# Performance work log

Hardware: AMD Instinct MI355X
Metric: run time of the kernel (lower is better)

## Reference

```python
import jax, jax.numpy as jnp
import numpy as np

B, N, DM, H, FF = 8, 2048, 1024, 16, 4096
D = DM // H // 2  # head_dim = 32
LAMBDA_INIT = 0.8 - 0.6 * float(np.exp(-0.3 * 1.0))  # layer_num=1


def _layernorm(x, g, b, eps=1e-5):
    mu = jnp.mean(x, axis=-1, keepdims=True)
    var = jnp.mean(jnp.square(x - mu), axis=-1, keepdims=True)
    return (x - mu) * jax.lax.rsqrt(var + eps) * g + b


def _rmsnorm(x, eps=1e-5):
    return x * jax.lax.rsqrt(jnp.mean(x * x, axis=-1, keepdims=True) + eps)


def _diff_attn(x, Wq, Wk, Wv, lq1, lq2, lk1, lk2, Wo, bo):
    b, n, d = x.shape
    scale = D ** -0.5
    # rearrange 'b n (h d q) -> b n (q h) d'
    q = (x @ Wq.T).reshape(b, n, H, D, 2).transpose(0, 1, 4, 2, 3).reshape(b, n, 2 * H, D) * scale
    k = (x @ Wk.T).reshape(b, n, H, D, 2).transpose(0, 1, 4, 2, 3).reshape(b, n, 2 * H, D)
    # rearrange 'b n (h d) -> b h n d' with d = 2*head_dim
    v = (x @ Wv.T).reshape(b, n, H, 2 * D).transpose(0, 2, 1, 3)
    # per-position head-vs-head scores: [b, n, 2H, 2H]
    att = jnp.einsum('bnqd,bnkd->bnqk', q, k)
    att = jnp.nan_to_num(att)
    att = jax.nn.softmax(att.astype(jnp.float32), axis=-1)
    lam = jnp.exp(jnp.sum(lq1 * lk1)) - jnp.exp(jnp.sum(lq2 * lk2)) + LAMBDA_INIT
    # rearrange 'b n (q h) (k a) -> q k b n h a'; take [0,0] - lam*[1,1]
    att6 = att.reshape(b, n, 2, H, 2, H)
    att2 = att6[:, :, 0, :, 0, :] - lam * att6[:, :, 1, :, 1, :]  # [b,n,h,a]
    out = jnp.einsum('bnah,bhnd->bnad', att2, v)  # [b,n,H,2D]
    out = _rmsnorm(out) * (1.0 - LAMBDA_INIT)
    out = out.reshape(b, n, d)
    return out @ Wo.T + bo


def setup_inputs() -> dict:
    key = jax.random.key(0)
    ks = jax.random.split(key, 12)
    p = lambda k, sh, s=0.02: jax.random.normal(k, sh, jnp.float32) * s
    return {
        'x': jax.random.normal(ks[0], (B, N, DM), jnp.float32),
        'Wq': p(ks[1], (DM, DM)), 'Wk': p(ks[2], (DM, DM)), 'Wv': p(ks[3], (DM, DM)),
        'lq1': p(ks[4], (D,), 0.1), 'lq2': p(ks[5], (D,), 0.1),
        'lk1': p(ks[6], (D,), 0.1), 'lk2': p(ks[7], (D,), 0.1),
        'Wo': p(ks[8], (DM, DM)), 'bo': jnp.zeros((DM,), jnp.float32),
        'ln1_g': jnp.ones((DM,), jnp.float32), 'ln1_b': jnp.zeros((DM,), jnp.float32),
        'ln2_g': jnp.ones((DM,), jnp.float32), 'ln2_b': jnp.zeros((DM,), jnp.float32),
        'W1': p(ks[9], (FF, DM)), 'b1': jnp.zeros((FF,), jnp.float32),
        'W2': p(ks[10], (DM, FF)), 'b2': jnp.zeros((DM,), jnp.float32),
    }


def reference(x, Wq, Wk, Wv, lq1, lq2, lk1, lk2, Wo, bo, ln1_g, ln1_b, ln2_g, ln2_b, W1, b1, W2, b2):
    # norm_first=True, use_gate=False, dropout=0 (eval), wo_ffn=False
    skip = x
    h = _layernorm(x, ln1_g, ln1_b)
    src2 = _diff_attn(h, Wq, Wk, Wv, lq1, lq2, lk1, lk2, Wo, bo)
    conn = skip + src2
    skip2 = conn
    h2 = _layernorm(conn, ln2_g, ln2_b)
    src3 = jax.nn.relu(h2 @ W1.T + b1) @ W2.T + b2
    return skip2 + src3
```

## Files before the change

### kernel.cpp

```cpp
#include <hip/hip_runtime.h>
#include <cstdint>

#define DM    1024
#define NHEAD 16
#define FFDIM 4096
#define MROWS 16384
#define QKVS  3072

static constexpr float LAMBDA_INIT_F = 0.3555090675909693f;
static constexpr float ONE_MINUS_LI  = 1.0f - 0.3555090675909693f;
static constexpr float QSCALE        = 0.17677669529663687f;

typedef __attribute__((ext_vector_type(8))) short bf16x8;
typedef __attribute__((ext_vector_type(4))) float f32x4;

__device__ __forceinline__ unsigned short f2bf(float f) {
    union { float f; unsigned int i; } w; w.f = f;
    unsigned int x = w.i;
    return (unsigned short)((x + 0x7fffu + ((x >> 16) & 1u)) >> 16);
}
__device__ __forceinline__ float bf2f(unsigned short u) {
    union { unsigned int i; float f; } w; w.i = ((unsigned int)u) << 16; return w.f;
}

__device__ __forceinline__ void load_lds16(const void* gptr, void* lptr) {
    __builtin_amdgcn_global_load_lds(
        (const __attribute__((address_space(1))) unsigned int*)gptr,
        (__attribute__((address_space(3))) unsigned int*)lptr, 16, 0, 0);
}

__global__ __launch_bounds__(256) void cvt6_kernel(const float* __restrict__ Wq,
                                                   const float* __restrict__ Wk,
                                                   const float* __restrict__ Wv,
                                                   const float* __restrict__ Wo,
                                                   const float* __restrict__ W1,
                                                   const float* __restrict__ W2,
                                                   unsigned short* __restrict__ wqkv,
                                                   unsigned short* __restrict__ wo,
                                                   unsigned short* __restrict__ w1,
                                                   unsigned short* __restrict__ w2)
{
    const int b = blockIdx.x;
    const float* src;
    unsigned short* dst;
    int off;
    if (b < 3072)      { src = (b < 1024) ? Wq : (b < 2048) ? Wk : Wv;
                         dst = wqkv + (b >> 10) * (DM * DM);
                         off = (b & 1023) * 1024; }
    else if (b < 4096) { src = Wo; dst = wo; off = (b - 3072) * 1024; }
    else if (b < 8192) { src = W1; dst = w1; off = (b - 4096) * 1024; }
    else               { src = W2; dst = w2; off = (b - 8192) * 1024; }
    const int i = off + threadIdx.x * 4;
    const float4 v = *(const float4*)&src[i];
    ushort4 o;
    o.x = f2bf(v.x); o.y = f2bf(v.y); o.z = f2bf(v.z); o.w = f2bf(v.w);
    *(ushort4*)&dst[i] = o;
}

__global__ __launch_bounds__(256) void ln_kernel(const float* __restrict__ xin,
                                                 const float* __restrict__ g,
                                                 const float* __restrict__ b,
                                                 unsigned short* __restrict__ out)
{
    const int row = blockIdx.x;
    const int tid = threadIdx.x;
    const int c0  = tid * 4;
    const float4 v = *(const float4*)&xin[(size_t)row * DM + c0];
    float s1 = v.x + v.y + v.z + v.w;
    float s2 = v.x*v.x + v.y*v.y + v.z*v.z + v.w*v.w;
    #pragma unroll
    for (int off = 32; off > 0; off >>= 1) {
        s1 += __shfl_down(s1, off);
        s2 += __shfl_down(s2, off);
    }
    __shared__ float red[8];
    const int wv = tid >> 6;
    if ((tid & 63) == 0) { red[wv] = s1; red[4 + wv] = s2; }
    __syncthreads();
    s1 = red[0] + red[1] + red[2] + red[3];
    s2 = red[4] + red[5] + red[6] + red[7];
    const float mean = s1 * (1.0f / DM);
    const float var  = s2 * (1.0f / DM) - mean * mean;
    const float inv  = rsqrtf(var + 1e-5f);
    const float4 g4 = *(const float4*)&g[c0];
    const float4 b4 = *(const float4*)&b[c0];
    ushort4 o;
    o.x = f2bf((v.x - mean) * inv * g4.x + b4.x);
    o.y = f2bf((v.y - mean) * inv * g4.y + b4.y);
    o.z = f2bf((v.z - mean) * inv * g4.z + b4.z);
    o.w = f2bf((v.w - mean) * inv * g4.w + b4.w);
    *(ushort4*)&out[(size_t)row * DM + c0] = o;
}

template<int EPI>
__global__ __launch_bounds__(512, 2) void gemm256(const unsigned short* __restrict__ A,
                                                  const unsigned short* __restrict__ W,
                                                  void* __restrict__ Cout,
                                                  const float* __restrict__ bias,
                                                  const float* __restrict__ resid,
                                                  int M, int N, int K, int ldb)
{
    __shared__ __align__(16) unsigned short Al[2][256][64];
    __shared__ __align__(16) unsigned short Bl[2][256][64];

    const int tid  = threadIdx.x;
    const int lane = tid & 63;
    const int wv   = tid >> 6;
    const int l15  = lane & 15;
    const int q4   = lane >> 4;
    const int wg   = wv >> 2;
    const int cg   = wv & 3;

    int bx = blockIdx.x, by = blockIdx.y;
    {
        const int gx  = gridDim.x;
        const int nwg = gx * gridDim.y;
        if ((nwg & 7) == 0) {
            const int lin = by * gx + bx;
            const int swz = (lin & 7) * (nwg >> 3) + (lin >> 3);
            bx = swz % gx;
            by = swz / gx;
        }
    }
    const int m0 = by * 256;
    const int n0 = bx * 256;
    const int KT = K >> 6;

    const int sr = tid >> 3;
    const int sc = (tid & 7) ^ (sr & 7);
    const unsigned short* gA = A + (size_t)(m0 + sr) * K   + sc * 8;
    const unsigned short* gB = W + (size_t)(n0 + sr) * ldb + sc * 8;
    const size_t aH = (size_t)128 * K;
    const size_t bH = (size_t)128 * ldb;
    const size_t aC = (size_t)64 * K;
    const size_t bC = (size_t)64 * ldb;
    unsigned short* lA = &Al[0][0][0] + wv * 512;
    unsigned short* lB = &Bl[0][0][0] + wv * 512;

#define STG_A(boff, hoff, gp) do { \
    load_lds16((gp),      lA + (boff) + (hoff)); \
    load_lds16((gp) + aC, lA + (boff) + (hoff) + 4096); } while (0)
#define STG_B(boff, hoff, gp) do { \
    load_lds16((gp),      lB + (boff) + (hoff)); \
    load_lds16((gp) + bC, lB + (boff) + (hoff) + 4096); } while (0)

    STG_A(0, 0,    gA);
    STG_B(0, 0,    gB);
    STG_A(0, 8192, gA + aH);
    STG_B(0, 8192, gB + bH);
    if (KT > 1) {
        STG_A(16384, 0,    gA + 64);
        STG_B(16384, 0,    gB + 64);
        STG_A(16384, 8192, gA + aH + 64);
        asm volatile("s_waitcnt vmcnt(6)" ::: "memory");
    } else {
        asm volatile("s_waitcnt vmcnt(0)" ::: "memory");
    }
    __builtin_amdgcn_s_barrier();
    __builtin_amdgcn_sched_barrier(0);

    const int so0 = ( q4      ^ (l15 & 7)) * 8;
    const int so1 = ((q4 + 4) ^ (l15 & 7)) * 8;
    const unsigned short* rA = &Al[0][wg * 64 + l15][0];
    const unsigned short* rB = &Bl[0][cg * 32 + l15][0];

    const f32x4 fz = {0.f, 0.f, 0.f, 0.f};
    f32x4 acc[8][4];
    #pragma unroll
    for (int i = 0; i < 8; ++i)
        #pragma unroll
        for (int j = 0; j < 4; ++j) acc[i][j] = fz;

    bf16x8 a[4][2], b0[2][2], b1[2][2];

    for (int t = 0; t < KT; ++t) {
        const int bo = (t & 1) << 14;
        const int bn = bo ^ 16384;
        const int k1 = (t + 1) << 6;
        const int k2 = (t + 2) << 6;

        a[0][0]  = *(const bf16x8*)&rA[bo + 0 * 1024 + so0];
        b0[0][0] = *(const bf16x8*)&rB[bo + 0 * 1024 + so0];
        a[0][1]  = *(const bf16x8*)&rA[bo + 0 * 1024 + so1];
        b0[0][1] = *(const bf16x8*)&rB[bo + 0 * 1024 + so1];
        b0[1][0] = *(const bf16x8*)&rB[bo + 1 * 1024 + so0];
        b0[1][1] = *(const bf16x8*)&rB[bo + 1 * 1024 + so1];
        a[1][0]  = *(const bf16x8*)&rA[bo + 1 * 1024 + so0];
        a[1][1]  = *(const bf16x8*)&rA[bo + 1 * 1024 + so1];
        a[2][0]  = *(const bf16x8*)&rA[bo + 2 * 1024 + so0];
        a[2][1]  = *(const bf16x8*)&rA[bo + 2 * 1024 + so1];
        a[3][0]  = *(const bf16x8*)&rA[bo + 3 * 1024 + so0];
        a[3][1]  = *(const bf16x8*)&rA[bo + 3 * 1024 + so1];
        if (t + 1 < KT) STG_B(bn, 8192, gB + bH + k1);
        __builtin_amdgcn_s_setprio(1);
        #pragma unroll
        for (int mf = 0; mf < 4; ++mf)
            #pragma unroll
            for (int nf = 0; nf < 2; ++nf) {
                acc[mf][nf] = __builtin_amdgcn_mfma_f32_16x16x32_bf16(a[mf][0], b0[nf][0], acc[mf][nf], 0, 0, 0);
                acc[mf][nf] = __builtin_amdgcn_mfma_f32_16x16x32_bf16(a[mf][1], b0[nf][1], acc[mf][nf], 0, 0, 0);
            }
        __builtin_amdgcn_s_setprio(0);
        __builtin_amdgcn_s_barrier();
        __builtin_amdgcn_sched_barrier(0);

        b1[0][0] = *(const bf16x8*)&rB[bo + 8192 + 0 * 1024 + so0];
        b1[0][1] = *(const bf16x8*)&rB[bo + 8192 + 0 * 1024 + so1];
        b1[1][0] = *(const bf16x8*)&rB[bo + 8192 + 1 * 1024 + so0];
        b1[1][1] = *(const bf16x8*)&rB[bo + 8192 + 1 * 1024 + so1];
        if (t + 2 < KT) STG_A(bo, 0, gA + k2);
        __builtin_amdgcn_s_setprio(1);
        #pragma unroll
        for (int mf = 0; mf < 4; ++mf)
            #pragma unroll
            for (int nf = 0; nf < 2; ++nf) {
                acc[mf][2 + nf] = __builtin_amdgcn_mfma_f32_16x16x32_bf16(a[mf][0], b1[nf][0], acc[mf][2 + nf], 0, 0, 0);
                acc[mf][2 + nf] = __builtin_amdgcn_mfma_f32_16x16x32_bf16(a[mf][1], b1[nf][1], acc[mf][2 + nf], 0, 0, 0);
            }
        __builtin_amdgcn_s_setprio(0);
        __builtin_amdgcn_s_barrier();
        __builtin_amdgcn_sched_barrier(0);

        a[0][0] = *(const bf16x8*)&rA[bo + 8192 + 0 * 1024 + so0];
        a[0][1] = *(const bf16x8*)&rA[bo + 8192 + 0 * 1024 + so1];
        a[1][0] = *(const bf16x8*)&rA[bo + 8192 + 1 * 1024 + so0];
        a[1][1] = *(const bf16x8*)&rA[bo + 8192 + 1 * 1024 + so1];
        a[2][0] = *(const bf16x8*)&rA[bo + 8192 + 2 * 1024 + so0];
        a[2][1] = *(const bf16x8*)&rA[bo + 8192 + 2 * 1024 + so1];
        a[3][0] = *(const bf16x8*)&rA[bo + 8192 + 3 * 1024 + so0];
        a[3][1] = *(const bf16x8*)&rA[bo + 8192 + 3 * 1024 + so1];
        if (t + 2 < KT) STG_B(bo, 0, gB + k2);
        __builtin_amdgcn_s_setprio(1);
        #pragma unroll
        for (int mf = 0; mf < 4; ++mf)
            #pragma unroll
            for (int nf = 0; nf < 2; ++nf) {
                acc[4 + mf][nf] = __builtin_amdgcn_mfma_f32_16x16x32_bf16(a[mf][0], b0[nf][0], acc[4 + mf][nf], 0, 0, 0);
                acc[4 + mf][nf] = __builtin_amdgcn_mfma_f32_16x16x32_bf16(a[mf][1], b0[nf][1], acc[4 + mf][nf], 0, 0, 0);
            }
        __builtin_amdgcn_s_setprio(0);
        __builtin_amdgcn_s_barrier();
        __builtin_amdgcn_sched_barrier(0);

        if (t + 2 < KT) STG_A(bo, 8192, gA + aH + k2);
        __builtin_amdgcn_s_setprio(1);
        #pragma unroll
        for (int mf = 0; mf < 4; ++mf)
            #pragma unroll
            for (int nf = 0; nf < 2; ++nf) {
                acc[4 + mf][2 + nf] = __builtin_amdgcn_mfma_f32_16x16x32_bf16(a[mf][0], b1[nf][0], acc[4 + mf][2 + nf], 0, 0, 0);
                acc[4 + mf][2 + nf] = __builtin_amdgcn_mfma_f32_16x16x32_bf16(a[mf][1], b1[nf][1], acc[4 + mf][2 + nf], 0, 0, 0);
            }
        __builtin_amdgcn_s_setprio(0);
        if (t + 2 < KT) {
            asm volatile("s_waitcnt vmcnt(6)" ::: "memory");
        } else if (t + 2 == KT) {
            asm volatile("s_waitcnt vmcnt(0)" ::: "memory");
        }
        if (t + 1 < KT) {
            __builtin_amdgcn_s_barrier();
            __builtin_amdgcn_sched_barrier(0);
        }
    }
#undef STG_A
#undef STG_B

    #pragma unroll
    for (int hm = 0; hm < 2; ++hm)
    #pragma unroll
    for (int mf = 0; mf < 4; ++mf)
    #pragma unroll
    for (int hb = 0; hb < 2; ++hb)
    #pragma unroll
    for (int nf = 0; nf < 2; ++nf)
    #pragma unroll
    for (int rr = 0; rr < 4; ++rr) {
        const int m = m0 + hm * 128 + wg * 64 + mf * 16 + q4 * 4 + rr;
        const int n = n0 + hb * 128 + cg * 32 + nf * 16 + l15;
        const size_t off = (size_t)m * N + n;
        float c = acc[hm * 4 + mf][hb * 2 + nf][rr];
        if (EPI == 0) {
            ((unsigned short*)Cout)[off] = f2bf(c);
        } else if (EPI == 1) {
            ((float*)Cout)[off] = c + bias[n] + resid[off];
        } else if (EPI == 2) {
            ((unsigned short*)Cout)[off] = f2bf(fmaxf(c + bias[n], 0.f));
        } else {
            ((float*)Cout)[off] = c + resid[off];
        }
    }
}

__global__ __launch_bounds__(256) void attn_pos(const unsigned short* __restrict__ qkv,
                                                const float* __restrict__ lq1,
                                                const float* __restrict__ lq2,
                                                const float* __restrict__ lk1,
                                                const float* __restrict__ lk2,
                                                unsigned short* __restrict__ outg)
{
    __shared__ __align__(16) float q2[4][32][36];
    __shared__ __align__(16) float k2[4][32][36];
    __shared__ __align__(16) float v2[4][16][64];
    __shared__ float att2[4][16][17];

    const int tid  = threadIdx.x;
    const int wave = tid >> 6;
    const int lane = tid & 63;
    const int pos  = blockIdx.x * 4 + wave;

    float s1 = 0.f, s2 = 0.f;
    #pragma unroll
    for (int i = 0; i < 32; ++i) {
        s1 += lq1[i] * lk1[i];
        s2 += lq2[i] * lk2[i];
    }
    const float lam = __expf(s1) - __expf(s2) + LAMBDA_INIT_F;

    const unsigned short* qrow = qkv + (size_t)pos * QKVS;
    const unsigned short* krow = qrow + DM;
    const unsigned short* vrow = qrow + 2 * DM;

    unsigned short tq[16], tk[16], tv[16];
    *(uint4*)&tq[0] = *(const uint4*)&qrow[lane * 16];
    *(uint4*)&tq[8] = *(const uint4*)&qrow[lane * 16 + 8];
    *(uint4*)&tk[0] = *(const uint4*)&krow[lane * 16];
    *(uint4*)&tk[8] = *(const uint4*)&krow[lane * 16 + 8];
    *(uint4*)&tv[0] = *(const uint4*)&vrow[lane * 16];
    *(uint4*)&tv[8] = *(const uint4*)&vrow[lane * 16 + 8];

    #pragma unroll
    for (int jj = 0; jj < 16; ++jj) {
        const int c  = lane * 16 + jj;
        const int h  = c >> 6;
        const int d  = (c >> 1) & 31;
        const int qi = c & 1;
        q2[wave][qi * 16 + h][d] = bf2f(tq[jj]) * QSCALE;
        k2[wave][qi * 16 + h][d] = bf2f(tk[jj]);
        v2[wave][c >> 6][c & 63] = bf2f(tv[jj]);
    }
    __syncthreads();

    const int qh = lane & 31, half = lane >> 5;
    float qreg[32];
    #pragma unroll
    for (int d4 = 0; d4 < 32; d4 += 4) {
        const f32x4 t = *(const f32x4*)&q2[wave][qh][d4];
        qreg[d4] = t[0]; qreg[d4+1] = t[1]; qreg[d4+2] = t[2]; qreg[d4+3] = t[3];
    }
    float p[16];
    #pragma unroll
    for (int jj = 0; jj < 16; ++jj) {
        const float* kr = &k2[wave][half * 16 + jj][0];
        float a = 0.f;
        #pragma unroll
        for (int d4 = 0; d4 < 32; d4 += 4) {
            const f32x4 kv = *(const f32x4*)&kr[d4];
            a += qreg[d4]*kv[0] + qreg[d4+1]*kv[1] + qreg[d4+2]*kv[2] + qreg[d4+3]*kv[3];
        }
        p[jj] = a;
    }

    float mx = p[0];
    #pragma unroll
    for (int jj = 1; jj < 16; ++jj) mx = fmaxf(mx, p[jj]);
    mx = fmaxf(mx, __shfl_xor(mx, 32));
    float sum = 0.f;
    #pragma unroll
    for (int jj = 0; jj < 16; ++jj) { p[jj] = __expf(p[jj] - mx); sum += p[jj]; }
    sum += __shfl_xor(sum, 32);
    const float inv = 1.0f / sum;

    if (half == 0 && qh < 16) {
        #pragma unroll
        for (int jj = 0; jj < 16; ++jj) att2[wave][qh][jj] = p[jj] * inv;
    }
    __syncthreads();
    if (half == 1 && qh >= 16) {
        const int a = qh - 16;
        #pragma unroll
        for (int jj = 0; jj < 16; ++jj) att2[wave][a][jj] -= lam * p[jj] * inv;
    }
    __syncthreads();

    const int a   = lane & 15;
    const int ddb = (lane >> 4) * 16;
    float areg[16];
    #pragma unroll
    for (int h = 0; h < 16; ++h) areg[h] = att2[wave][a][h];
    float o[16];
    #pragma unroll
    for (int j = 0; j < 16; ++j) o[j] = 0.f;
    #pragma unroll
    for (int h = 0; h < 16; ++h) {
        #pragma unroll
        for (int j4 = 0; j4 < 16; j4 += 4) {
            const f32x4 vv = *(const f32x4*)&v2[wave][h][ddb + j4];
            o[j4]   += areg[h] * vv[0];
            o[j4+1] += areg[h] * vv[1];
            o[j4+2] += areg[h] * vv[2];
            o[j4+3] += areg[h] * vv[3];
        }
    }

    float ss = 0.f;
    #pragma unroll
    for (int j = 0; j < 16; ++j) ss += o[j] * o[j];
    ss += __shfl_xor(ss, 16);
    ss += __shfl_xor(ss, 32);
    const float scl = rsqrtf(ss * (1.0f / 64.0f) + 1e-5f) * ONE_MINUS_LI;

    unsigned short ob[16];
    #pragma unroll
    for (int j = 0; j < 16; ++j) ob[j] = f2bf(o[j] * scl);
    unsigned short* orow = outg + (size_t)pos * DM + a * 64 + ddb;
    *(uint4*)&orow[0] = *(const uint4*)&ob[0];
    *(uint4*)&orow[8] = *(const uint4*)&ob[8];
}

extern "C" void kernel_launch(void* const* d_in, const int* in_sizes, int n_in,
                              void* d_out, int out_size, void* d_ws, size_t ws_size,
                              hipStream_t stream)
{
    const float* x   = (const float*)d_in[0];
    const float* Wq  = (const float*)d_in[1];
    const float* Wk  = (const float*)d_in[2];
    const float* Wv  = (const float*)d_in[3];
    const float* lq1 = (const float*)d_in[4];
    const float* lq2 = (const float*)d_in[5];
    const float* lk1 = (const float*)d_in[6];
    const float* lk2 = (const float*)d_in[7];
    const float* Wo  = (const float*)d_in[8];
    const float* bo  = (const float*)d_in[9];
    const float* g1  = (const float*)d_in[10];
    const float* be1 = (const float*)d_in[11];
    const float* g2  = (const float*)d_in[12];
    const float* be2 = (const float*)d_in[13];
    const float* W1  = (const float*)d_in[14];
    const float* b1  = (const float*)d_in[15];
    const float* W2  = (const float*)d_in[16];
    const float* b2  = (const float*)d_in[17];
    (void)in_sizes; (void)n_in; (void)out_size;

    const size_t MB = 1ull << 20;
    char* ws = (char*)d_ws;
    unsigned short* wqkv = (unsigned short*)(ws);
    unsigned short* wo   = (unsigned short*)(ws + 6 * MB);
    unsigned short* w1   = (unsigned short*)(ws + 8 * MB);
    unsigned short* w2   = (unsigned short*)(ws + 16 * MB);
    unsigned short* h    = (unsigned short*)(ws + 24 * MB);
    unsigned short* qkv  = (unsigned short*)(ws + 56 * MB);
    float*          conn = (float*)(ws + 56 * MB);
    unsigned short* attn = h;
    unsigned short* h2   = h;
    unsigned short* t    = (unsigned short*)(ws + 120 * MB);

    int nf = 1;
    while (nf < 16 && 120 * MB + (size_t)MROWS * (FFDIM / nf) * 2 > ws_size) nf <<= 1;
    const int FC = FFDIM / nf;

    const dim3 b256(256), b512(512);

    cvt6_kernel<<<12288, b256, 0, stream>>>(Wq, Wk, Wv, Wo, W1, W2, wqkv, wo, w1, w2);

    ln_kernel<<<MROWS, b256, 0, stream>>>(x, g1, be1, h);

    gemm256<0><<<dim3(QKVS / 256, MROWS / 256), b512, 0, stream>>>(
        h, wqkv, qkv, nullptr, nullptr, MROWS, QKVS, DM, DM);

    attn_pos<<<MROWS / 4, b256, 0, stream>>>(qkv, lq1, lq2, lk1, lk2, attn);

    gemm256<1><<<dim3(DM / 256, MROWS / 256), b512, 0, stream>>>(
        attn, wo, conn, bo, x, MROWS, DM, DM, DM);

    ln_kernel<<<MROWS, b256, 0, stream>>>(conn, g2, be2, h2);

    for (int c = 0; c < nf; ++c) {
        gemm256<2><<<dim3(FC / 256, MROWS / 256), b512, 0, stream>>>(
            h2, w1 + (size_t)c * FC * DM, t, b1 + c * FC, nullptr, MROWS, FC, DM, DM);
        if (c == 0)
            gemm256<1><<<dim3(DM / 256, MROWS / 256), b512, 0, stream>>>(
                t, w2 + (size_t)c * FC, (float*)d_out, b2, conn, MROWS, DM, FC, FFDIM);
        else
            gemm256<4><<<dim3(DM / 256, MROWS / 256), b512, 0, stream>>>(
                t, w2 + (size_t)c * FC, (float*)d_out, nullptr, (const float*)d_out, MROWS, DM, FC, FFDIM);
    }
}
```

Measured before the change: 665.0 us.

## Use bf16 MFMA for per-position head attention, drop block syncs

Rewrites the per-position differential attention kernel so the 32x32 Q·K scores and the 16x16·16x64 attention-times-V product run on bf16 MFMA instructions instead of scalar fp32 FMAs. Q, K and V stay in bf16 in shared memory, with V transposed and zero padded so the K=32 MFMA can consume it. Block-wide __syncthreads are replaced by wave-local lgkmcnt waits, since each wave owns its own position. The trade-off is that the softmax probabilities are rounded to bf16 before the V product, and the kernel is a small part of a larger pipeline dominated by GEMMs.

Measured after the change: 669.2 us. About the same (+0.6%).

```diff
diff --git a/kernel.cpp b/kernel.cpp
--- a/kernel.cpp
+++ b/kernel.cpp
@@ -298,14 +298,17 @@
                                                 const float* __restrict__ lk2,
                                                 unsigned short* __restrict__ outg)
 {
-    __shared__ __align__(16) float q2[4][32][36];
-    __shared__ __align__(16) float k2[4][32][36];
-    __shared__ __align__(16) float v2[4][16][64];
-    __shared__ float att2[4][16][17];
+    __shared__ __align__(16) unsigned short qs[4][32][32];
+    __shared__ __align__(16) unsigned short ks[4][32][32];
+    __shared__ __align__(16) unsigned short vt[4][64][40];
+    __shared__ __align__(16) unsigned short at[4][16][40];
+    __shared__ __align__(16) unsigned short ot[4][1024];
 
     const int tid  = threadIdx.x;
     const int wave = tid >> 6;
     const int lane = tid & 63;
+    const int l15  = lane & 15;
+    const int q4   = lane >> 4;
     const int pos  = blockIdx.x * 4 + wave;
 
     float s1 = 0.f, s2 = 0.f;
@@ -317,104 +320,120 @@
     const float lam = __expf(s1) - __expf(s2) + LAMBDA_INIT_F;
 
     const unsigned short* qrow = qkv + (size_t)pos * QKVS;
-    const unsigned short* krow = qrow + DM;
-    const unsigned short* vrow = qrow + 2 * DM;
-
-    unsigned short tq[16], tk[16], tv[16];
-    *(uint4*)&tq[0] = *(const uint4*)&qrow[lane * 16];
-    *(uint4*)&tq[8] = *(const uint4*)&qrow[lane * 16 + 8];
-    *(uint4*)&tk[0] = *(const uint4*)&krow[lane * 16];
-    *(uint4*)&tk[8] = *(const uint4*)&krow[lane * 16 + 8];
-    *(uint4*)&tv[0] = *(const uint4*)&vrow[lane * 16];
-    *(uint4*)&tv[8] = *(const uint4*)&vrow[lane * 16 + 8];
-
-    #pragma unroll
-    for (int jj = 0; jj < 16; ++jj) {
-        const int c  = lane * 16 + jj;
-        const int h  = c >> 6;
-        const int d  = (c >> 1) & 31;
-        const int qi = c & 1;
-        q2[wave][qi * 16 + h][d] = bf2f(tq[jj]) * QSCALE;
-        k2[wave][qi * 16 + h][d] = bf2f(tk[jj]);
-        v2[wave][c >> 6][c & 63] = bf2f(tv[jj]);
-    }
-    __syncthreads();
-
-    const int qh = lane & 31, half = lane >> 5;
-    float qreg[32];
-    #pragma unroll
-    for (int d4 = 0; d4 < 32; d4 += 4) {
-        const f32x4 t = *(const f32x4*)&q2[wave][qh][d4];
-        qreg[d4] = t[0]; qreg[d4+1] = t[1]; qreg[d4+2] = t[2]; qreg[d4+3] = t[3];
-    }
-    float p[16];
-    #pragma unroll
-    for (int jj = 0; jj < 16; ++jj) {
-        const float* kr = &k2[wave][half * 16 + jj][0];
-        float a = 0.f;
-        #pragma unroll
-        for (int d4 = 0; d4 < 32; d4 += 4) {
-            const f32x4 kv = *(const f32x4*)&kr[d4];
-            a += qreg[d4]*kv[0] + qreg[d4+1]*kv[1] + qreg[d4+2]*kv[2] + qreg[d4+3]*kv[3];
+    const uint4 uq0 = *(const uint4*)&qrow[lane * 16];
+    const uint4 uq1 = *(const uint4*)&qrow[lane * 16 + 8];
+    const uint4 uk0 = *(const uint4*)&qrow[DM + lane * 16];
+    const uint4 uk1 = *(const uint4*)&qrow[DM + lane * 16 + 8];
+    const uint4 uv0 = *(const uint4*)&qrow[2 * DM + lane * 16];
+    const uint4 uv1 = *(const uint4*)&qrow[2 * DM + lane * 16 + 8];
+
+    const int h  = lane >> 2;
+    const int d0 = (lane & 3) * 8;
+#define LO16(a, b) (((a) & 0xffffu) | ((b) << 16))
+#define HI16(a, b) (((a) >> 16) | ((b) & 0xffff0000u))
+    {
+        uint4 e, o;
+        e.x = LO16(uq0.x, uq0.y); e.y = LO16(uq0.z, uq0.w);
+        e.z = LO16(uq1.x, uq1.y); e.w = LO16(uq1.z, uq1.w);
+        o.x = HI16(uq0.x, uq0.y); o.y = HI16(uq0.z, uq0.w);
+        o.z = HI16(uq1.x, uq1.y); o.w = HI16(uq1.z, uq1.w);
+        *(uint4*)&qs[wave][h][d0]      = e;
+        *(uint4*)&qs[wave][16 + h][d0] = o;
+        e.x = LO16(uk0.x, uk0.y); e.y = LO16(uk0.z, uk0.w);
+        e.z = LO16(uk1.x, uk1.y); e.w = LO16(uk1.z, uk1.w);
+        o.x = HI16(uk0.x, uk0.y); o.y = HI16(uk0.z, uk0.w);
+        o.z = HI16(uk1.x, uk1.y); o.w = HI16(uk1.z, uk1.w);
+        *(uint4*)&ks[wave][h][d0]      = e;
+        *(uint4*)&ks[wave][16 + h][d0] = o;
+    }
+#undef LO16
+#undef HI16
+    {
+        unsigned short tv[16];
+        *(uint4*)&tv[0] = uv0;
+        *(uint4*)&tv[8] = uv1;
+        const int ddb0 = (lane & 3) * 16;
+        #pragma unroll
+        for (int j = 0; j < 16; ++j) vt[wave][ddb0 + j][h] = tv[j];
+    }
+    {
+        const uint4 z4 = {0u, 0u, 0u, 0u};
+        *(uint4*)&vt[wave][lane][16] = z4;
+        *(uint4*)&vt[wave][lane][24] = z4;
+        *(uint4*)&at[wave][l15][16]  = z4;
+        *(uint4*)&at[wave][l15][24]  = z4;
+    }
+    asm volatile("s_waitcnt lgkmcnt(0)" ::: "memory");
+    __builtin_amdgcn_sched_barrier(0);
+
+    const f32x4 fz = {0.f, 0.f, 0.f, 0.f};
+    const bf16x8 a0 = *(const bf16x8*)&qs[wave][l15][q4 * 8];
+    const bf16x8 a1 = *(const bf16x8*)&qs[wave][16 + l15][q4 * 8];
+    const bf16x8 k0 = *(const bf16x8*)&ks[wave][l15][q4 * 8];
+    const bf16x8 k1 = *(const bf16x8*)&ks[wave][16 + l15][q4 * 8];
+    f32x4 t00 = __builtin_amdgcn_mfma_f32_16x16x32_bf16(a0, k0, fz, 0, 0, 0);
+    f32x4 t01 = __builtin_amdgcn_mfma_f32_16x16x32_bf16(a0, k1, fz, 0, 0, 0);
+    f32x4 t10 = __builtin_amdgcn_mfma_f32_16x16x32_bf16(a1, k0, fz, 0, 0, 0);
+    f32x4 t11 = __builtin_amdgcn_mfma_f32_16x16x32_bf16(a1, k1, fz, 0, 0, 0);
+
+    float p00[4], p11[4], i0[4], i1[4];
+    #pragma unroll
+    for (int r = 0; r < 4; ++r) {
+        const float s00 = t00[r] * QSCALE, s01 = t01[r] * QSCALE;
+        const float s10 = t10[r] * QSCALE, s11 = t11[r] * QSCALE;
+        float m0 = fmaxf(s00, s01);
+        float m1 = fmaxf(s10, s11);
+        #pragma unroll
+        for (int mk = 1; mk < 16; mk <<= 1) {
+            m0 = fmaxf(m0, __shfl_xor(m0, mk));
+            m1 = fmaxf(m1, __shfl_xor(m1, mk));
         }
-        p[jj] = a;
-    }
-
-    float mx = p[0];
-    #pragma unroll
-    for (int jj = 1; jj < 16; ++jj) mx = fmaxf(mx, p[jj]);
-    mx = fmaxf(mx, __shfl_xor(mx, 32));
-    float sum = 0.f;
-    #pragma unroll
-    for (int jj = 0; jj < 16; ++jj) { p[jj] = __expf(p[jj] - mx); sum += p[jj]; }
-    sum += __shfl_xor(sum, 32);
-    const float inv = 1.0f / sum;
-
-    if (half == 0 && qh < 16) {
-        #pragma unroll
-        for (int jj = 0; jj < 16; ++jj) att2[wave][qh][jj] = p[jj] * inv;
-    }
-    __syncthreads();
-    if (half == 1 && qh >= 16) {
-        const int a = qh - 16;
-        #pragma unroll
-        for (int jj = 0; jj < 16; ++jj) att2[wave][a][jj] -= lam * p[jj] * inv;
-    }
-    __syncthreads();
-
-    const int a   = lane & 15;
-    const int ddb = (lane >> 4) * 16;
-    float areg[16];
-    #pragma unroll
-    for (int h = 0; h < 16; ++h) areg[h] = att2[wave][a][h];
-    float o[16];
-    #pragma unroll
-    for (int j = 0; j < 16; ++j) o[j] = 0.f;
-    #pragma unroll
-    for (int h = 0; h < 16; ++h) {
-        #pragma unroll
-        for (int j4 = 0; j4 < 16; j4 += 4) {
-            const f32x4 vv = *(const f32x4*)&v2[wave][h][ddb + j4];
-            o[j4]   += areg[h] * vv[0];
-            o[j4+1] += areg[h] * vv[1];
-            o[j4+2] += areg[h] * vv[2];
-            o[j4+3] += areg[h] * vv[3];
+        p00[r] = __expf(s00 - m0);
+        const float q01 = __expf(s01 - m0);
+        const float q10 = __expf(s10 - m1);
+        p11[r] = __expf(s11 - m1);
+        float u0 = p00[r] + q01;
+        float u1 = q10 + p11[r];
+        #pragma unroll
+        for (int mk = 1; mk < 16; mk <<= 1) {
+            u0 += __shfl_xor(u0, mk);
+            u1 += __shfl_xor(u1, mk);
         }
-    }
-
-    float ss = 0.f;
-    #pragma unroll
-    for (int j = 0; j < 16; ++j) ss += o[j] * o[j];
-    ss += __shfl_xor(ss, 16);
-    ss += __shfl_xor(ss, 32);
-    const float scl = rsqrtf(ss * (1.0f / 64.0f) + 1e-5f) * ONE_MINUS_LI;
-
-    unsigned short ob[16];
-    #pragma unroll
-    for (int j = 0; j < 16; ++j) ob[j] = f2bf(o[j] * scl);
-    unsigned short* orow = outg + (size_t)pos * DM + a * 64 + ddb;
-    *(uint4*)&orow[0] = *(const uint4*)&ob[0];
-    *(uint4*)&orow[8] = *(const uint4*)&ob[8];
+        i0[r] = 1.0f / u0;
+        i1[r] = 1.0f / u1;
+    }
+    #pragma unroll
+    for (int r = 0; r < 4; ++r) {
+        const float v = p00[r] * i0[r] - lam * p11[r] * i1[r];
+        at[wave][q4 * 4 + r][l15] = f2bf(v);
+    }
+    asm volatile("s_waitcnt lgkmcnt(0)" ::: "memory");
+    __builtin_amdgcn_sched_barrier(0);
+
+    const bf16x8 pa = *(const bf16x8*)&at[wave][l15][q4 * 8];
+    f32x4 o0 = __builtin_amdgcn_mfma_f32_16x16x32_bf16(pa, *(const bf16x8*)&vt[wave][ 0 + l15][q4 * 8], fz, 0, 0, 0);
+    f32x4 o1 = __builtin_amdgcn_mfma_f32_16x16x32_bf16(pa, *(const bf16x8*)&vt[wave][16 + l15][q4 * 8], fz, 0, 0, 0);
+    f32x4 o2 = __builtin_amdgcn_mfma_f32_16x16x32_bf16(pa, *(const bf16x8*)&vt[wave][32 + l15][q4 * 8], fz, 0, 0, 0);
+    f32x4 o3 = __builtin_amdgcn_mfma_f32_16x16x32_bf16(pa, *(const bf16x8*)&vt[wave][48 + l15][q4 * 8], fz, 0, 0, 0);
+
+    #pragma unroll
+    for (int r = 0; r < 4; ++r) {
+        float ss = o0[r]*o0[r] + o1[r]*o1[r] + o2[r]*o2[r] + o3[r]*o3[r];
+        #pragma unroll
+        for (int mk = 1; mk < 16; mk <<= 1) ss += __shfl_xor(ss, mk);
+        const float scl = rsqrtf(ss * (1.0f / 64.0f) + 1e-5f) * ONE_MINUS_LI;
+        const int a = q4 * 4 + r;
+        ot[wave][a * 64 +  0 + l15] = f2bf(o0[r] * scl);
+        ot[wave][a * 64 + 16 + l15] = f2bf(o1[r] * scl);
+        ot[wave][a * 64 + 32 + l15] = f2bf(o2[r] * scl);
+        ot[wave][a * 64 + 48 + l15] = f2bf(o3[r] * scl);
+    }
+    asm volatile("s_waitcnt lgkmcnt(0)" ::: "memory");
+    __builtin_amdgcn_sched_barrier(0);
+
+    unsigned short* orow = outg + (size_t)pos * DM;
+    *(uint4*)&orow[lane * 16]     = *(const uint4*)&ot[wave][lane * 16];
+    *(uint4*)&orow[lane * 16 + 8] = *(const uint4*)&ot[wave][lane * 16 + 8];
 }
 
 extern "C" void kernel_launch(void* const* d_in, const int* in_sizes, int n_in,
```
